# Kernel optimization log

Hardware: AMD Instinct MI355X
Metric: run time of the kernel (lower is better)

## Reference

```python
import jax, jax.numpy as jnp
import numpy as np

LN_EPS = 1e-5


def setup_inputs() -> dict:
    key = jax.random.key(0)
    ks = jax.random.split(key, 12)
    B, T, U, H, V = 4, 512, 128, 512, 41
    src = jax.random.normal(ks[0], (B, T, H), dtype=jnp.float32)
    tgt = jax.random.normal(ks[1], (B, U, H), dtype=jnp.float32)
    src_len = jax.random.randint(ks[2], (B,), 1, T + 1, dtype=jnp.int32)
    tgt_len = jax.random.randint(ks[3], (B,), 1, U + 1, dtype=jnp.int32)
    s = 1.0 / np.sqrt(H)
    W1 = jax.random.uniform(ks[4], (H, H), jnp.float32, -s, s)
    b1 = jax.random.uniform(ks[5], (H,), jnp.float32, -s, s)
    W2 = jax.random.uniform(ks[6], (H, H), jnp.float32, -s, s)
    b2 = jax.random.uniform(ks[7], (H,), jnp.float32, -s, s)
    ln_g = jnp.ones((H,), jnp.float32)
    ln_b = jnp.zeros((H,), jnp.float32)
    Wl = jax.random.uniform(ks[8], (H, V), jnp.float32, -s, s)
    bl = jax.random.uniform(ks[9], (V,), jnp.float32, -s, s)
    return dict(source_encodings=src, source_lengths=src_len,
                target_encodings=tgt, target_lengths=tgt_len,
                W1=W1, b1=b1, W2=W2, b2=b2, ln_g=ln_g, ln_b=ln_b,
                Wl=Wl, bl=bl)


def _f_target(tgt, W1, b1, W2, b2, ln_g, ln_b):
    h = jax.nn.gelu(tgt @ W1 + b1, approximate=False)  # exact GELU (torch default)
    h = h @ W2 + b2
    mu = jnp.mean(h, axis=-1, keepdims=True)
    var = jnp.var(h, axis=-1, keepdims=True)
    return (h - mu) * jax.lax.rsqrt(var + LN_EPS) * ln_g + ln_b


def reference(source_encodings, source_lengths, target_encodings, target_lengths,
              W1, b1, W2, b2, ln_g, ln_b, Wl, bl):
    tgt = _f_target(target_encodings, W1, b1, W2, b2, ln_g, ln_b)  # [B,U,H]
    # joint broadcast add: [B,T,1,H] + [B,1,U,H] -> [B,T,U,H]
    joint = source_encodings[:, :, None, :] + tgt[:, None, :, :]
    act = jnp.tanh(joint)
    out = act @ Wl + bl  # [B,T,U,V]
    return out, source_lengths, target_lengths
```

## Files before the change

kernel.cpp:

```cpp
#include <hip/hip_runtime.h>
#include <math.h>

#define Bb 4
#define Tt 512
#define Uu 128
#define Hh 512
#define Vv 41

typedef __attribute__((ext_vector_type(8))) short short8;
typedef __attribute__((ext_vector_type(4))) float f32x4;
typedef __attribute__((ext_vector_type(2))) float v2f;

__device__ __forceinline__ unsigned pack_bf16_rne(float hi, float lo) {
    unsigned xh = __float_as_uint(hi); xh += 0x7fffu + ((xh >> 16) & 1u);
    unsigned xl = __float_as_uint(lo); xl += 0x7fffu + ((xl >> 16) & 1u);
    return __builtin_amdgcn_perm(xh, xl, 0x07060302);
}

__device__ __forceinline__ unsigned short bf16_rne(float v) {
    unsigned x = __float_as_uint(v);
    x += 0x7fffu + ((x >> 16) & 1u);
    return (unsigned short)(x >> 16);
}

__device__ __forceinline__ float bf16lo(unsigned u) { return __uint_as_float(u << 16); }
__device__ __forceinline__ float bf16hi(unsigned u) { return __uint_as_float(u & 0xffff0000u); }

__device__ __forceinline__ float tanh_acc(float x) {
    float e = __expf(2.0f * x);
    return 1.0f - 2.0f * __builtin_amdgcn_rcpf(e + 1.0f);
}

__device__ __forceinline__ unsigned mob2p(v2f tt, v2f ts) {
    v2f nm = ts + tt;
    v2f dn = ts * tt + (v2f){1.f, 1.f};
    float r = __builtin_amdgcn_rcpf(dn.x * dn.y);
    v2f q = nm * (v2f){dn.y, dn.x};
    v2f g = q * (v2f){r, r};
    return __builtin_amdgcn_perm(__float_as_uint(g.y), __float_as_uint(g.x), 0x07060302);
}

__global__ __launch_bounds__(256) void prep_pack(
    const float* __restrict__ W1, const float* __restrict__ W2,
    const float* __restrict__ Wl, const float* __restrict__ tgt,
    unsigned short* __restrict__ Wp1, unsigned short* __restrict__ Wp2,
    unsigned short* __restrict__ Wpl3, unsigned short* __restrict__ tgtA,
    const int* __restrict__ sl, const int* __restrict__ tl,
    float* __restrict__ lenDst)
{
    __shared__ __align__(16) char smem[16640];
    const int bid = blockIdx.x, tid = threadIdx.x;

    if (bid >= 136) {
        unsigned short (*At)[520] = (unsigned short (*)[520])smem;
        const int rt = bid - 136;
        const float4* t4 = (const float4*)(tgt + (size_t)rt * 16 * Hh);
        #pragma unroll
        for (int j = 0; j < 8; ++j) {
            int fi = j * 256 + tid;
            int row = fi >> 7, c4 = fi & 127;
            float4 v = t4[fi];
            uint2 pk;
            pk.x = pack_bf16_rne(v.y, v.x);
            pk.y = pack_bf16_rne(v.w, v.z);
            *(uint2*)&At[row][c4 * 4] = pk;
        }
        __syncthreads();
        #pragma unroll
        for (int i = 0; i < 4; ++i) {
            int chunk = i * 256 + tid;
            int ks = chunk >> 6, l = chunk & 63;
            int q = l >> 4, nc = l & 15;
            short8 v = *(const short8*)&At[nc][ks * 32 + q * 8];
            *(short8*)(tgtA + ((size_t)(rt * 16 + ks) * 64 + l) * 8) = v;
        }
        return;
    }

    if (bid == 135 && tid < 2 * Bb)
        lenDst[tid] = (tid < Bb) ? (float)sl[tid] : (float)tl[tid - Bb];

    float (*T)[65] = (float (*)[65])smem;
    const float* Wsrc; unsigned short* Wdst; int k0, n0, isWl;
    if (bid < 64)       { Wsrc = W1; Wdst = Wp1; k0 = (bid >> 3) * 64; n0 = (bid & 7) * 64; isWl = 0; }
    else if (bid < 128) { Wsrc = W2; Wdst = Wp2; k0 = ((bid - 64) >> 3) * 64; n0 = ((bid - 64) & 7) * 64; isWl = 0; }
    else                { Wsrc = Wl; Wdst = Wpl3; k0 = (bid - 128) * 64; n0 = 0; isWl = 1; }

    #pragma unroll
    for (int i = 0; i < 16; ++i) {
        int idx = i * 256 + tid;
        int kk = idx >> 6, nn = idx & 63;
        float v;
        if (isWl) v = (nn < Vv) ? Wl[(k0 + kk) * Vv + nn] : 0.0f;
        else      v = Wsrc[(size_t)(k0 + kk) * 512 + n0 + nn];
        T[kk][nn] = v;
    }
    __syncthreads();

    #pragma unroll
    for (int i = 0; i < 2; ++i) {
        int task = i * 256 + tid;
        int nn = task & 63, kg = task >> 6;
        if (isWl && nn >= 48) continue;
        int n = n0 + nn, k = k0 + kg * 8;
        float e[8];
        #pragma unroll
        for (int j = 0; j < 8; ++j) e[j] = T[kg * 8 + j][nn];
        uint4 pk;
        pk.x = pack_bf16_rne(e[1], e[0]);
        pk.y = pack_bf16_rne(e[3], e[2]);
        pk.z = pack_bf16_rne(e[5], e[4]);
        pk.w = pack_bf16_rne(e[7], e[6]);
        int ntg = n >> 4, ncol = n & 15;
        int ks = (k >> 5) & 15, quad = (k >> 3) & 3;
        int lane = quad * 16 + ncol;
        size_t slot = isWl ? (size_t)((ks * 3 + ntg) * 64 + lane)
                           : (size_t)((ntg * 16 + ks) * 64 + lane);
        *(uint4*)(Wdst + slot * 8) = pk;
    }
}

__global__ __launch_bounds__(512) void target_fused(
    const unsigned short* __restrict__ tgtA,
    const unsigned short* __restrict__ Wp1, const float* __restrict__ b1,
    const unsigned short* __restrict__ Wp2, const float* __restrict__ b2,
    const float* __restrict__ ln_g, const float* __restrict__ ln_b,
    unsigned short* __restrict__ tgtPb)
{
    __shared__ unsigned short At[16][520];
    __shared__ float Ct[16][520];

    const int rt = blockIdx.x;
    const int tid = threadIdx.x, lane = tid & 63, w = tid >> 6;
    const int ncol = lane & 15, quad = lane >> 4;

    const unsigned short* ap = tgtA + ((size_t)rt * 1024 + lane) * 8;
    const unsigned short* bp1 = Wp1 + (size_t)lane * 8 + (size_t)(w * 4) * 8192;
    const unsigned short* bp2 = Wp2 + (size_t)lane * 8 + (size_t)(w * 4) * 8192;

    f32x4 acc[4];
    #pragma unroll
    for (int i = 0; i < 4; ++i) acc[i] = (f32x4){0.f, 0.f, 0.f, 0.f};

    {
        short8 ac = *(const short8*)(ap);
        short8 bc[4];
        #pragma unroll
        for (int i = 0; i < 4; ++i) bc[i] = *(const short8*)(bp1 + (size_t)i * 8192);
        #pragma unroll
        for (int ks = 0; ks < 16; ++ks) {
            short8 an, bn[4];
            if (ks < 15) {
                an = *(const short8*)(ap + (ks + 1) * 512);
                #pragma unroll
                for (int i = 0; i < 4; ++i)
                    bn[i] = *(const short8*)(bp1 + (size_t)i * 8192 + (ks + 1) * 512);
            }
            #pragma unroll
            for (int i = 0; i < 4; ++i)
                acc[i] = __builtin_amdgcn_mfma_f32_16x16x32_bf16(ac, bc[i], acc[i], 0, 0, 0);
            ac = an;
            #pragma unroll
            for (int i = 0; i < 4; ++i) bc[i] = bn[i];
        }
    }

    #pragma unroll
    for (int nt = 0; nt < 4; ++nt) {
        int n = w * 64 + nt * 16 + ncol;
        float bias = b1[n];
        #pragma unroll
        for (int r = 0; r < 4; ++r) {
            float v = acc[nt][r] + bias;
            float g = 0.5f * v * (1.0f + erff(v * 0.70710678118654752f));
            At[quad * 4 + r][n] = bf16_rne(g);
        }
        acc[nt] = (f32x4){0.f, 0.f, 0.f, 0.f};
    }
    __syncthreads();

    {
        short8 bc[4];
        #pragma unroll
        for (int i = 0; i < 4; ++i) bc[i] = *(const short8*)(bp2 + (size_t)i * 8192);
        #pragma unroll
        for (int ks = 0; ks < 16; ++ks) {
            short8 bn[4];
            if (ks < 15) {
                #pragma unroll
                for (int i = 0; i < 4; ++i)
                    bn[i] = *(const short8*)(bp2 + (size_t)i * 8192 + (ks + 1) * 512);
            }
            short8 af = *(const short8*)&At[ncol][ks * 32 + quad * 8];
            #pragma unroll
            for (int i = 0; i < 4; ++i)
                acc[i] = __builtin_amdgcn_mfma_f32_16x16x32_bf16(af, bc[i], acc[i], 0, 0, 0);
            #pragma unroll
            for (int i = 0; i < 4; ++i) bc[i] = bn[i];
        }
    }

    #pragma unroll
    for (int nt = 0; nt < 4; ++nt) {
        int n = w * 64 + nt * 16 + ncol;
        float bias = b2[n];
        #pragma unroll
        for (int r = 0; r < 4; ++r)
            Ct[quad * 4 + r][n] = acc[nt][r] + bias;
    }
    __syncthreads();

    #pragma unroll
    for (int rr = 0; rr < 2; ++rr) {
        const int row = w * 2 + rr;
        const float4* cr = (const float4*)&Ct[row][0];
        float4 v0 = cr[lane], v1 = cr[lane + 64];
        float s = v0.x + v0.y + v0.z + v0.w + v1.x + v1.y + v1.z + v1.w;
        float q = v0.x*v0.x + v0.y*v0.y + v0.z*v0.z + v0.w*v0.w
                + v1.x*v1.x + v1.y*v1.y + v1.z*v1.z + v1.w*v1.w;
        #pragma unroll
        for (int off = 32; off > 0; off >>= 1) {
            s += __shfl_xor(s, off, 64);
            q += __shfl_xor(q, off, 64);
        }
        float mu = s * (1.0f / Hh);
        float rs = rsqrtf(q * (1.0f / Hh) - mu * mu + 1e-5f);

        const int r = rt * 16 + row;
        const int bb = r >> 7, u = r & 127;
        #pragma unroll
        for (int j = 0; j < 2; ++j) {
            int k0 = j * 256 + lane * 4;
            float4 v = j ? v1 : v0;
            float4 g4 = ((const float4*)ln_g)[j * 64 + lane];
            float4 b4 = ((const float4*)ln_b)[j * 64 + lane];
            float4 o;
            o.x = tanh_acc((v.x - mu) * rs * g4.x + b4.x);
            o.y = tanh_acc((v.y - mu) * rs * g4.y + b4.y);
            o.z = tanh_acc((v.z - mu) * rs * g4.z + b4.z);
            o.w = tanh_acc((v.w - mu) * rs * g4.w + b4.w);
            uint2 pk;
            pk.x = pack_bf16_rne(o.y, o.x);
            pk.y = pack_bf16_rne(o.w, o.z);
            int chunk = k0 >> 3, half = (k0 >> 2) & 1;
            *(uint2*)(tgtPb + ((size_t)(bb * 64 + chunk) * 128 + u) * 8 + half * 4) = pk;
        }
    }
}

__global__ __launch_bounds__(256) void joint_mfma(
    const float* __restrict__ src, const unsigned short* __restrict__ tgtPb,
    const unsigned short* __restrict__ Wpl3, const float* __restrict__ bl,
    float* __restrict__ out)
{
    __shared__ float srcl[2 * Hh];
    __shared__ __align__(16) float tileC[64 * Vv];

    const int t0 = blockIdx.x * 2, b = blockIdx.y, uh = blockIdx.z;
    const int tid = threadIdx.x;
    const int lane = tid & 63, wave = tid >> 6;
    const int ncol = lane & 15, quad = lane >> 4;

    {
        const float4* s4 = (const float4*)(src + ((size_t)(b * Tt + t0)) * Hh);
        float4 v = s4[tid];
        v.x = tanh_acc(v.x); v.y = tanh_acc(v.y);
        v.z = tanh_acc(v.z); v.w = tanh_acc(v.w);
        ((float4*)srcl)[tid] = v;
    }

    const int u0 = uh * 64 + wave * 16 + ncol;
    const unsigned short* apl = tgtPb + (size_t)b * 65536 + ((size_t)quad * 128 + u0) * 8;
    const unsigned short* bpl = Wpl3 + (size_t)lane * 8;

    uint4 Aq[2];
    short8 Bq[2][3];
    Aq[0] = *(const uint4*)(apl);
    Bq[0][0] = *(const short8*)(bpl);
    Bq[0][1] = *(const short8*)(bpl + 512);
    Bq[0][2] = *(const short8*)(bpl + 1024);
    apl += 4096; bpl += 1536;
    Aq[1] = *(const uint4*)(apl);
    Bq[1][0] = *(const short8*)(bpl);
    Bq[1][1] = *(const short8*)(bpl + 512);
    Bq[1][2] = *(const short8*)(bpl + 1024);
    apl += 4096; bpl += 1536;

    f32x4 acc[2][3];
    #pragma unroll
    for (int nt = 0; nt < 3; ++nt) {
        int n = nt * 16 + ncol;
        float bv = (n < Vv) ? bl[n] : 0.0f;
        acc[0][nt] = (f32x4){bv, bv, bv, bv};
        acc[1][nt] = (f32x4){bv, bv, bv, bv};
    }

    __syncthreads();
    const float* sr0 = srcl;
    const float* sr1 = srcl + Hh;
    float4 sA0 = *(const float4*)(sr0 + quad * 8);
    float4 sB0 = *(const float4*)(sr0 + quad * 8 + 4);
    float4 sA1 = *(const float4*)(sr1 + quad * 8);
    float4 sB1 = *(const float4*)(sr1 + quad * 8 + 4);

    #pragma unroll
    for (int ks = 0; ks < 16; ++ks) {
        const int st = ks & 1;
        uint4 a = Aq[st];
        short8 B0 = Bq[st][0], B1 = Bq[st][1], B2 = Bq[st][2];

        if (ks + 2 < 16) {
            Aq[st] = *(const uint4*)(apl);
            Bq[st][0] = *(const short8*)(bpl);
            Bq[st][1] = *(const short8*)(bpl + 512);
            Bq[st][2] = *(const short8*)(bpl + 1024);
            apl += 4096; bpl += 1536;
        }
        float4 nsA0, nsB0, nsA1, nsB1;
        if (ks < 15) {
            const int o = (ks + 1) * 32 + quad * 8;
            nsA0 = *(const float4*)(sr0 + o);
            nsB0 = *(const float4*)(sr0 + o + 4);
            nsA1 = *(const float4*)(sr1 + o);
            nsB1 = *(const float4*)(sr1 + o + 4);
        }

        __builtin_amdgcn_sched_barrier(0);

        v2f tA = {bf16lo(a.x), bf16hi(a.x)};
        v2f tB = {bf16lo(a.y), bf16hi(a.y)};
        v2f tC = {bf16lo(a.z), bf16hi(a.z)};
        v2f tD = {bf16lo(a.w), bf16hi(a.w)};

        union { uint4 u; short8 s; } f0, f1;
        f0.u.x = mob2p(tA, (v2f){sA0.x, sA0.y});
        f0.u.y = mob2p(tB, (v2f){sA0.z, sA0.w});
        f0.u.z = mob2p(tC, (v2f){sB0.x, sB0.y});
        f0.u.w = mob2p(tD, (v2f){sB0.z, sB0.w});
        f1.u.x = mob2p(tA, (v2f){sA1.x, sA1.y});
        f1.u.y = mob2p(tB, (v2f){sA1.z, sA1.w});
        f1.u.z = mob2p(tC, (v2f){sB1.x, sB1.y});
        f1.u.w = mob2p(tD, (v2f){sB1.z, sB1.w});

        acc[0][0] = __builtin_amdgcn_mfma_f32_16x16x32_bf16(f0.s, B0, acc[0][0], 0, 0, 0);
        acc[1][0] = __builtin_amdgcn_mfma_f32_16x16x32_bf16(f1.s, B0, acc[1][0], 0, 0, 0);
        acc[0][1] = __builtin_amdgcn_mfma_f32_16x16x32_bf16(f0.s, B1, acc[0][1], 0, 0, 0);
        acc[1][1] = __builtin_amdgcn_mfma_f32_16x16x32_bf16(f1.s, B1, acc[1][1], 0, 0, 0);
        acc[0][2] = __builtin_amdgcn_mfma_f32_16x16x32_bf16(f0.s, B2, acc[0][2], 0, 0, 0);
        acc[1][2] = __builtin_amdgcn_mfma_f32_16x16x32_bf16(f1.s, B2, acc[1][2], 0, 0, 0);

        sA0 = nsA0; sB0 = nsB0; sA1 = nsA1; sB1 = nsB1;
    }

    #pragma unroll
    for (int t = 0; t < 2; ++t) {
        if (t) __syncthreads();
        #pragma unroll
        for (int nt = 0; nt < 3; ++nt) {
            int n = nt * 16 + ncol;
            if (n < Vv) {
                #pragma unroll
                for (int r = 0; r < 4; ++r)
                    tileC[(wave * 16 + quad * 4 + r) * Vv + n] = acc[t][nt][r];
            }
        }
        __syncthreads();
        float* ob = out + (((size_t)(b * Tt + t0 + t)) * Uu + uh * 64) * Vv;
        const float4* tc4 = (const float4*)tileC;
        #pragma unroll
        for (int i = 0; i < 3; ++i) {
            int idx = i * 256 + tid;
            if (idx < 656)
                ((float4*)ob)[idx] = tc4[idx];
        }
    }
}

extern "C" void kernel_launch(void* const* d_in, const int* in_sizes, int n_in,
                              void* d_out, int out_size, void* d_ws, size_t ws_size,
                              hipStream_t stream)
{
    const float* src  = (const float*)d_in[0];
    const int*   slen = (const int*)  d_in[1];
    const float* tgt  = (const float*)d_in[2];
    const int*   tlen = (const int*)  d_in[3];
    const float* W1   = (const float*)d_in[4];
    const float* b1   = (const float*)d_in[5];
    const float* W2   = (const float*)d_in[6];
    const float* b2   = (const float*)d_in[7];
    const float* ln_g = (const float*)d_in[8];
    const float* ln_b = (const float*)d_in[9];
    const float* Wl   = (const float*)d_in[10];
    const float* bl   = (const float*)d_in[11];

    float* out = (float*)d_out;
    char* ws = (char*)d_ws;
    unsigned short* tgtPb = (unsigned short*)(ws);
    unsigned short* Wp1   = (unsigned short*)(ws + 524288);
    unsigned short* Wp2   = (unsigned short*)(ws + 1048576);
    unsigned short* Wpl3  = (unsigned short*)(ws + 1572864);
    unsigned short* tgtA  = (unsigned short*)(ws + 1638400);

    hipLaunchKernelGGL(prep_pack, dim3(168), dim3(256), 0, stream,
                       W1, W2, Wl, tgt, Wp1, Wp2, Wpl3, tgtA,
                       slen, tlen, out + (size_t)Bb * Tt * Uu * Vv);
    hipLaunchKernelGGL(target_fused, dim3(32), dim3(512), 0, stream,
                       tgtA, Wp1, b1, Wp2, b2, ln_g, ln_b, tgtPb);
    hipLaunchKernelGGL(joint_mfma, dim3(Tt / 2, Bb, 2), dim3(256), 0, stream,
                       src, tgtPb, Wpl3, bl, out);
}
```

Before: 134.9 us.

## Switch joint tanh-addition math and MFMA from fp32/bf16 to packed fp16

The joint kernel combines tanh(src) and tanh(tgt) with the tanh addition formula. This moves that combination from fp32 v2f math plus bf16 packing to packed half2 arithmetic (hadd2, hfma2, h2rcp), and feeds fp16 MFMA instead of bf16. Wl and the target activations are now packed as fp16, and the source tanh values are stored in LDS as packed halves, which halves LDS traffic and cuts ALU work per element. The cost is reduced dynamic range and a lower-precision reciprocal, which could affect accuracy, and the sched_barrier is removed.

```diff
diff --git a/kernel.cpp b/kernel.cpp
--- a/kernel.cpp
+++ b/kernel.cpp
@@ -1,4 +1,5 @@
 #include <hip/hip_runtime.h>
+#include <hip/hip_fp16.h>
 #include <math.h>
 
 #define Bb 4
@@ -9,7 +10,7 @@
 
 typedef __attribute__((ext_vector_type(8))) short short8;
 typedef __attribute__((ext_vector_type(4))) float f32x4;
-typedef __attribute__((ext_vector_type(2))) float v2f;
+typedef _Float16 half8 __attribute__((ext_vector_type(8)));
 
 __device__ __forceinline__ unsigned pack_bf16_rne(float hi, float lo) {
     unsigned xh = __float_as_uint(hi); xh += 0x7fffu + ((xh >> 16) & 1u);
@@ -23,21 +24,26 @@
     return (unsigned short)(x >> 16);
 }
 
-__device__ __forceinline__ float bf16lo(unsigned u) { return __uint_as_float(u << 16); }
-__device__ __forceinline__ float bf16hi(unsigned u) { return __uint_as_float(u & 0xffff0000u); }
+__device__ __forceinline__ unsigned pkh(float lo, float hi) {
+    auto p = __builtin_amdgcn_cvt_pkrtz(lo, hi);
+    union { decltype(p) h; unsigned u; } c;
+    c.h = p;
+    return c.u;
+}
 
 __device__ __forceinline__ float tanh_acc(float x) {
     float e = __expf(2.0f * x);
     return 1.0f - 2.0f * __builtin_amdgcn_rcpf(e + 1.0f);
 }
 
-__device__ __forceinline__ unsigned mob2p(v2f tt, v2f ts) {
-    v2f nm = ts + tt;
-    v2f dn = ts * tt + (v2f){1.f, 1.f};
-    float r = __builtin_amdgcn_rcpf(dn.x * dn.y);
-    v2f q = nm * (v2f){dn.y, dn.x};
-    v2f g = q * (v2f){r, r};
-    return __builtin_amdgcn_perm(__float_as_uint(g.y), __float_as_uint(g.x), 0x07060302);
+__device__ __forceinline__ unsigned mobh(unsigned ttu, unsigned tsu) {
+    union U { unsigned u; __half2 h; };
+    U a, s, g;
+    a.u = ttu; s.u = tsu;
+    __half2 nm = __hadd2(s.h, a.h);
+    __half2 dn = __hfma2(s.h, a.h, __float2half2_rn(1.0f));
+    g.h = __hmul2(nm, h2rcp(dn));
+    return g.u;
 }
 
 __global__ __launch_bounds__(256) void prep_pack(
@@ -107,10 +113,17 @@
         #pragma unroll
         for (int j = 0; j < 8; ++j) e[j] = T[kg * 8 + j][nn];
         uint4 pk;
-        pk.x = pack_bf16_rne(e[1], e[0]);
-        pk.y = pack_bf16_rne(e[3], e[2]);
-        pk.z = pack_bf16_rne(e[5], e[4]);
-        pk.w = pack_bf16_rne(e[7], e[6]);
+        if (isWl) {
+            pk.x = pkh(e[0], e[1]);
+            pk.y = pkh(e[2], e[3]);
+            pk.z = pkh(e[4], e[5]);
+            pk.w = pkh(e[6], e[7]);
+        } else {
+            pk.x = pack_bf16_rne(e[1], e[0]);
+            pk.y = pack_bf16_rne(e[3], e[2]);
+            pk.z = pack_bf16_rne(e[5], e[4]);
+            pk.w = pack_bf16_rne(e[7], e[6]);
+        }
         int ntg = n >> 4, ncol = n & 15;
         int ks = (k >> 5) & 15, quad = (k >> 3) & 3;
         int lane = quad * 16 + ncol;
@@ -240,8 +253,8 @@
             o.z = tanh_acc((v.z - mu) * rs * g4.z + b4.z);
             o.w = tanh_acc((v.w - mu) * rs * g4.w + b4.w);
             uint2 pk;
-            pk.x = pack_bf16_rne(o.y, o.x);
-            pk.y = pack_bf16_rne(o.w, o.z);
+            pk.x = pkh(o.x, o.y);
+            pk.y = pkh(o.z, o.w);
             int chunk = k0 >> 3, half = (k0 >> 2) & 1;
             *(uint2*)(tgtPb + ((size_t)(bb * 64 + chunk) * 128 + u) * 8 + half * 4) = pk;
         }
@@ -253,7 +266,7 @@
     const unsigned short* __restrict__ Wpl3, const float* __restrict__ bl,
     float* __restrict__ out)
 {
-    __shared__ float srcl[2 * Hh];
+    __shared__ __align__(16) unsigned srclh[2 * 256];
     __shared__ __align__(16) float tileC[64 * Vv];
 
     const int t0 = blockIdx.x * 2, b = blockIdx.y, uh = blockIdx.z;
@@ -266,24 +279,26 @@
         float4 v = s4[tid];
         v.x = tanh_acc(v.x); v.y = tanh_acc(v.y);
         v.z = tanh_acc(v.z); v.w = tanh_acc(v.w);
-        ((float4*)srcl)[tid] = v;
+        srclh[2 * tid]     = pkh(v.x, v.y);
+        srclh[2 * tid + 1] = pkh(v.z, v.w);
     }
 
     const int u0 = uh * 64 + wave * 16 + ncol;
     const unsigned short* apl = tgtPb + (size_t)b * 65536 + ((size_t)quad * 128 + u0) * 8;
     const unsigned short* bpl = Wpl3 + (size_t)lane * 8;
 
+    union HF { uint4 u; half8 h; };
     uint4 Aq[2];
-    short8 Bq[2][3];
+    HF Bq[2][3];
     Aq[0] = *(const uint4*)(apl);
-    Bq[0][0] = *(const short8*)(bpl);
-    Bq[0][1] = *(const short8*)(bpl + 512);
-    Bq[0][2] = *(const short8*)(bpl + 1024);
+    Bq[0][0].u = *(const uint4*)(bpl);
+    Bq[0][1].u = *(const uint4*)(bpl + 512);
+    Bq[0][2].u = *(const uint4*)(bpl + 1024);
     apl += 4096; bpl += 1536;
     Aq[1] = *(const uint4*)(apl);
-    Bq[1][0] = *(const short8*)(bpl);
-    Bq[1][1] = *(const short8*)(bpl + 512);
-    Bq[1][2] = *(const short8*)(bpl + 1024);
+    Bq[1][0].u = *(const uint4*)(bpl);
+    Bq[1][1].u = *(const uint4*)(bpl + 512);
+    Bq[1][2].u = *(const uint4*)(bpl + 1024);
     apl += 4096; bpl += 1536;
 
     f32x4 acc[2][3];
@@ -296,60 +311,46 @@
     }
 
     __syncthreads();
-    const float* sr0 = srcl;
-    const float* sr1 = srcl + Hh;
-    float4 sA0 = *(const float4*)(sr0 + quad * 8);
-    float4 sB0 = *(const float4*)(sr0 + quad * 8 + 4);
-    float4 sA1 = *(const float4*)(sr1 + quad * 8);
-    float4 sB1 = *(const float4*)(sr1 + quad * 8 + 4);
+    uint4 s0 = *(const uint4*)&srclh[quad * 4];
+    uint4 s1 = *(const uint4*)&srclh[256 + quad * 4];
 
     #pragma unroll
     for (int ks = 0; ks < 16; ++ks) {
         const int st = ks & 1;
         uint4 a = Aq[st];
-        short8 B0 = Bq[st][0], B1 = Bq[st][1], B2 = Bq[st][2];
+        HF B0 = Bq[st][0], B1 = Bq[st][1], B2 = Bq[st][2];
 
         if (ks + 2 < 16) {
             Aq[st] = *(const uint4*)(apl);
-            Bq[st][0] = *(const short8*)(bpl);
-            Bq[st][1] = *(const short8*)(bpl + 512);
-            Bq[st][2] = *(const short8*)(bpl + 1024);
+            Bq[st][0].u = *(const uint4*)(bpl);
+            Bq[st][1].u = *(const uint4*)(bpl + 512);
+            Bq[st][2].u = *(const uint4*)(bpl + 1024);
             apl += 4096; bpl += 1536;
         }
-        float4 nsA0, nsB0, nsA1, nsB1;
+        uint4 ns0, ns1;
         if (ks < 15) {
-            const int o = (ks + 1) * 32 + quad * 8;
-            nsA0 = *(const float4*)(sr0 + o);
-            nsB0 = *(const float4*)(sr0 + o + 4);
-            nsA1 = *(const float4*)(sr1 + o);
-            nsB1 = *(const float4*)(sr1 + o + 4);
-        }
-
-        __builtin_amdgcn_sched_barrier(0);
-
-        v2f tA = {bf16lo(a.x), bf16hi(a.x)};
-        v2f tB = {bf16lo(a.y), bf16hi(a.y)};
-        v2f tC = {bf16lo(a.z), bf16hi(a.z)};
-        v2f tD = {bf16lo(a.w), bf16hi(a.w)};
-
-        union { uint4 u; short8 s; } f0, f1;
-        f0.u.x = mob2p(tA, (v2f){sA0.x, sA0.y});
-        f0.u.y = mob2p(tB, (v2f){sA0.z, sA0.w});
-        f0.u.z = mob2p(tC, (v2f){sB0.x, sB0.y});
-        f0.u.w = mob2p(tD, (v2f){sB0.z, sB0.w});
-        f1.u.x = mob2p(tA, (v2f){sA1.x, sA1.y});
-        f1.u.y = mob2p(tB, (v2f){sA1.z, sA1.w});
-        f1.u.z = mob2p(tC, (v2f){sB1.x, sB1.y});
-        f1.u.w = mob2p(tD, (v2f){sB1.z, sB1.w});
-
-        acc[0][0] = __builtin_amdgcn_mfma_f32_16x16x32_bf16(f0.s, B0, acc[0][0], 0, 0, 0);
-        acc[1][0] = __builtin_amdgcn_mfma_f32_16x16x32_bf16(f1.s, B0, acc[1][0], 0, 0, 0);
-        acc[0][1] = __builtin_amdgcn_mfma_f32_16x16x32_bf16(f0.s, B1, acc[0][1], 0, 0, 0);
-        acc[1][1] = __builtin_amdgcn_mfma_f32_16x16x32_bf16(f1.s, B1, acc[1][1], 0, 0, 0);
-        acc[0][2] = __builtin_amdgcn_mfma_f32_16x16x32_bf16(f0.s, B2, acc[0][2], 0, 0, 0);
-        acc[1][2] = __builtin_amdgcn_mfma_f32_16x16x32_bf16(f1.s, B2, acc[1][2], 0, 0, 0);
-
-        sA0 = nsA0; sB0 = nsB0; sA1 = nsA1; sB1 = nsB1;
+            ns0 = *(const uint4*)&srclh[(ks + 1) * 16 + quad * 4];
+            ns1 = *(const uint4*)&srclh[256 + (ks + 1) * 16 + quad * 4];
+        }
+
+        HF f0, f1;
+        f0.u.x = mobh(a.x, s0.x);
+        f0.u.y = mobh(a.y, s0.y);
+        f0.u.z = mobh(a.z, s0.z);
+        f0.u.w = mobh(a.w, s0.w);
+        f1.u.x = mobh(a.x, s1.x);
+        f1.u.y = mobh(a.y, s1.y);
+        f1.u.z = mobh(a.z, s1.z);
+        f1.u.w = mobh(a.w, s1.w);
+
+        acc[0][0] = __builtin_amdgcn_mfma_f32_16x16x32_f16(f0.h, B0.h, acc[0][0], 0, 0, 0);
+        acc[1][0] = __builtin_amdgcn_mfma_f32_16x16x32_f16(f1.h, B0.h, acc[1][0], 0, 0, 0);
+        acc[0][1] = __builtin_amdgcn_mfma_f32_16x16x32_f16(f0.h, B1.h, acc[0][1], 0, 0, 0);
+        acc[1][1] = __builtin_amdgcn_mfma_f32_16x16x32_f16(f1.h, B1.h, acc[1][1], 0, 0, 0);
+        acc[0][2] = __builtin_amdgcn_mfma_f32_16x16x32_f16(f0.h, B2.h, acc[0][2], 0, 0, 0);
+        acc[1][2] = __builtin_amdgcn_mfma_f32_16x16x32_f16(f1.h, B2.h, acc[1][2], 0, 0, 0);
+
+        s0 = ns0; s1 = ns1;
     }
 
     #pragma unroll
```

Result: no change. 135.1 us (+0.1%).
